# Performance work log

Measured on AMD Instinct MI355X. Metric: run time of the kernel, lower is better.

Reference implementation:

```python
import jax, jax.numpy as jnp
import numpy as np

N_NODES = 50000
N_EDGES = 800000
IN_DIM = 128
OUT_DIM = 128
N_CLASSES = 10
N_GRAPHS = 64


def setup_inputs() -> dict:
    key = jax.random.key(0)
    ks = jax.random.split(key, 8)
    features = jax.random.normal(ks[0], (N_NODES, IN_DIM), dtype=jnp.float32)
    src = jax.random.randint(ks[1], (N_EDGES,), 0, N_NODES, dtype=jnp.int64)
    dst = jax.random.randint(ks[2], (N_EDGES,), 0, N_NODES, dtype=jnp.int64)
    graph_ids = jnp.sort(jax.random.randint(ks[3], (N_NODES,), 0, N_GRAPHS, dtype=jnp.int64))
    # GraphConv params (glorot-ish scale) and linear head params
    W = jax.random.normal(ks[4], (IN_DIM, OUT_DIM), dtype=jnp.float32) / np.sqrt(IN_DIM)
    b = jnp.zeros((OUT_DIM,), dtype=jnp.float32)
    W_head = jax.random.normal(ks[5], (OUT_DIM, N_CLASSES), dtype=jnp.float32) / np.sqrt(OUT_DIM)
    b_head = jnp.zeros((N_CLASSES,), dtype=jnp.float32)
    return {"features": features, "src": src, "dst": dst, "graph_ids": graph_ids,
            "W": W, "b": b, "W_head": W_head, "b_head": b_head}


def reference(features, src, dst, graph_ids, W, b, W_head, b_head):
    # DGL GraphConv, norm='both': D_out^-1/2 -> sum aggregate -> D_in^-1/2 -> XW+b -> relu
    ones_e = jnp.ones((src.shape[0],), dtype=features.dtype)
    out_deg = jax.ops.segment_sum(ones_e, src, num_segments=N_NODES)
    in_deg = jax.ops.segment_sum(ones_e, dst, num_segments=N_NODES)
    out_norm = jax.lax.rsqrt(jnp.clip(out_deg, 1.0))[:, None]   # [N,1]
    in_norm = jax.lax.rsqrt(jnp.clip(in_deg, 1.0))[:, None]     # [N,1]
    h = features * out_norm                                      # [N,D]
    agg = jax.ops.segment_sum(h[src], dst, num_segments=N_NODES) # gather-scatter [E,D]->[N,D]
    agg = agg * in_norm
    h = jax.nn.relu(agg @ W + b)                                 # [N,D_out]
    # dgl.mean_nodes: segment mean over graphs (note: original returns after layer 0)
    cnt = jax.ops.segment_sum(jnp.ones((N_NODES,), dtype=h.dtype), graph_ids, num_segments=N_GRAPHS)
    pooled = jax.ops.segment_sum(h, graph_ids, num_segments=N_GRAPHS) / jnp.clip(cnt, 1.0)[:, None]
    return pooled @ W_head + b_head                              # [G, n_classes]
```

## Files before the change

### kernel.cpp

```cpp
#include <hip/hip_runtime.h>

#define N_NODES   50000
#define N_EDGES   800000
#define DIM       128
#define N_GRAPHS  64
#define N_CLASSES 10
#define NCHE      64
#define CSZ       (N_EDGES / NCHE)
#define LQ        (N_NODES / 4)
#define WPB       64
#define NBR2      ((LQ + WPB - 1) / WPB)
#define PLACE_BPC ((CSZ + 255) / 256)
#define PLACE_BLKS (NCHE * PLACE_BPC)
#define PRES_BLKS ((N_NODES * DIM / 8 + 255) / 256)
#define WT_BLKS   (DIM * DIM / 256)
#define NPBM      128
#define NBLK_NODE ((N_NODES + NPBM - 1) / NPBM)

typedef _Float16 h8 __attribute__((ext_vector_type(8)));
typedef float f4v __attribute__((ext_vector_type(4)));

__global__ __launch_bounds__(256) void k_lhist(const int* __restrict__ src,
                                               const int* __restrict__ dst,
                                               unsigned* __restrict__ Hin,
                                               unsigned* __restrict__ Hout,
                                               unsigned char* __restrict__ perm) {
    __shared__ unsigned L[LQ];
    int c = blockIdx.x, t = threadIdx.x;
    int base = c * CSZ;
    for (int w = t; w < LQ; w += 256) L[w] = 0u;
    __syncthreads();
    if (blockIdx.y == 0) {
        for (int i = t; i < CSZ; i += 256) {
            int d = dst[base + i];
            int sh = (d & 3) * 8;
            unsigned old = atomicAdd(&L[d >> 2], 1u << sh);
            perm[base + i] = (unsigned char)((old >> sh) & 0xffu);
        }
        __syncthreads();
        for (int w = t; w < LQ; w += 256) Hin[(size_t)c * LQ + w] = L[w];
    } else {
        for (int i = t; i < CSZ; i += 256) {
            int s = src[base + i];
            atomicAdd(&L[s >> 2], 1u << ((s & 3) * 8));
        }
        __syncthreads();
        for (int w = t; w < LQ; w += 256) Hout[(size_t)c * LQ + w] = L[w];
    }
}

__global__ __launch_bounds__(256) void k_reduce(unsigned* __restrict__ Hin,
                                                const unsigned* __restrict__ Hout,
                                                const int* __restrict__ gid,
                                                unsigned* __restrict__ indeg,
                                                float* __restrict__ outnorm,
                                                float* __restrict__ innorm,
                                                int* __restrict__ start,
                                                unsigned* __restrict__ row_ptr,
                                                unsigned* __restrict__ blockSums) {
    __shared__ unsigned sIn[4][WPB];
    __shared__ unsigned sOut[4][WPB];
    __shared__ unsigned sS[WPB];
    int t = threadIdx.x;
    int wl = t & (WPB - 1);
    int g  = t >> 6;
    int w  = blockIdx.x * WPB + wl;
    unsigned gs = 0, os = 0;
    int c0 = g * (NCHE / 4);
    if (w < LQ) {
        for (int c = c0; c < c0 + NCHE / 4; ++c) {
            gs += Hin[(size_t)c * LQ + w];
            os += Hout[(size_t)c * LQ + w];
        }
    }
    sIn[g][wl] = gs; sOut[g][wl] = os;
    __syncthreads();
    unsigned baseg = 0;
    for (int gg = 0; gg < 4; ++gg) if (gg < g) baseg += sIn[gg][wl];
    if (w < LQ) {
        unsigned running = baseg;
        for (int c = c0; c < c0 + NCHE / 4; ++c) {
            size_t idx = (size_t)c * LQ + w;
            unsigned word = Hin[idx];
            Hin[idx] = running;
            running += word;
        }
    }
    unsigned tot = 0, otot = 0, wtot = 0;
    if (t < WPB) {
        tot  = sIn[0][t] + sIn[1][t] + sIn[2][t] + sIn[3][t];
        otot = sOut[0][t] + sOut[1][t] + sOut[2][t] + sOut[3][t];
        wtot = (tot & 0xffu) + ((tot >> 8) & 0xffu) + ((tot >> 16) & 0xffu) + (tot >> 24);
        sS[t] = wtot;
    }
    __syncthreads();
    for (int off = 1; off < WPB; off <<= 1) {
        unsigned x = (t < WPB && t >= off) ? sS[t - off] : 0u;
        __syncthreads();
        if (t < WPB) sS[t] += x;
        __syncthreads();
    }
    if (t < WPB) {
        int ww = blockIdx.x * WPB + t;
        if (ww < LQ) {
            unsigned r0 = tot & 0xffu, r1 = (tot >> 8) & 0xffu,
                     r2 = (tot >> 16) & 0xffu, r3 = tot >> 24;
            unsigned o0 = otot & 0xffu, o1 = (otot >> 8) & 0xffu,
                     o2 = (otot >> 16) & 0xffu, o3 = otot >> 24;
            unsigned ex = sS[t] - wtot;
            int n = 4 * ww;
            row_ptr[n]     = ex;
            row_ptr[n + 1] = ex + r0;
            row_ptr[n + 2] = ex + r0 + r1;
            row_ptr[n + 3] = ex + r0 + r1 + r2;
            unsigned rr[4] = {r0, r1, r2, r3}, oo[4] = {o0, o1, o2, o3};
#pragma unroll
            for (int j = 0; j < 4; ++j) {
                indeg[n + j]   = rr[j];
                innorm[n + j]  = rsqrtf(fmaxf((float)rr[j], 1.0f));
                outnorm[n + j] = rsqrtf(fmaxf((float)oo[j], 1.0f));
                int i = n + j;
                int gq = gid[i];
                if (i == 0) {
                    for (int x2 = 0; x2 <= gq; ++x2) start[x2] = 0;
                } else {
                    int gp = gid[i - 1];
                    if (gp != gq)
                        for (int x2 = gp + 1; x2 <= gq; ++x2) start[x2] = i;
                }
                if (i == N_NODES - 1)
                    for (int x2 = gq + 1; x2 <= N_GRAPHS; ++x2) start[x2] = N_NODES;
            }
        }
        if (t == WPB - 1) blockSums[blockIdx.x] = sS[WPB - 1];
    }
}

__global__ __launch_bounds__(256) void k_scan2(unsigned* __restrict__ blockSums,
                                               unsigned* __restrict__ blockOff,
                                               float* __restrict__ pooled) {
    __shared__ unsigned s[256];
    int t = threadIdx.x;
    unsigned val = (t < NBR2) ? blockSums[t] : 0u;
    s[t] = val;
    __syncthreads();
    for (int off = 1; off < 256; off <<= 1) {
        unsigned x = (t >= off) ? s[t - off] : 0u;
        __syncthreads();
        s[t] += x;
        __syncthreads();
    }
    if (t < NBR2) blockOff[t] = s[t] - val;
    float4 z = {0.f, 0.f, 0.f, 0.f};
    for (int i = t; i < N_GRAPHS * DIM / 4; i += 256)
        reinterpret_cast<float4*>(pooled)[i] = z;
}

__global__ __launch_bounds__(256) void k_prep(const int* __restrict__ src,
                                              const int* __restrict__ dst,
                                              const unsigned* __restrict__ Hin,
                                              const unsigned char* __restrict__ perm,
                                              const unsigned* __restrict__ row_ptr,
                                              const unsigned* __restrict__ blockOff,
                                              unsigned short* __restrict__ bsrc,
                                              const float* __restrict__ feat,
                                              const float* __restrict__ outnorm,
                                              _Float16* __restrict__ sfeat,
                                              const float* __restrict__ W,
                                              _Float16* __restrict__ Wt) {
    int t = threadIdx.x;
    int blk = blockIdx.x;
    if (blk < PLACE_BLKS) {
        int c = blk / PLACE_BPC;
        int i = (blk % PLACE_BPC) * 256 + t;
        if (i < CSZ) {
            int e = c * CSZ + i;
            int d = dst[e];
            int sh = (d & 3) * 8;
            unsigned pre = (Hin[(size_t)c * LQ + (d >> 2)] >> sh) & 0xffu;
            unsigned pos = row_ptr[d] + blockOff[d >> 8] + pre + perm[e];
            bsrc[pos] = (unsigned short)src[e];
        }
    } else if (blk < PLACE_BLKS + PRES_BLKS) {
        int i = (blk - PLACE_BLKS) * 256 + t;
        if (i < N_NODES * DIM / 8) {
            int n = i >> 4;
            int d = (i & 15) << 3;
            float nrm = outnorm[n];
            const float4* p = reinterpret_cast<const float4*>(feat + (size_t)n * DIM + d);
            float4 a = p[0], q = p[1];
            h8 r;
            r[0] = (_Float16)(a.x * nrm); r[1] = (_Float16)(a.y * nrm);
            r[2] = (_Float16)(a.z * nrm); r[3] = (_Float16)(a.w * nrm);
            r[4] = (_Float16)(q.x * nrm); r[5] = (_Float16)(q.y * nrm);
            r[6] = (_Float16)(q.z * nrm); r[7] = (_Float16)(q.w * nrm);
            *reinterpret_cast<h8*>(sfeat + (size_t)n * DIM + d) = r;
        }
    } else {
        int i = (blk - PLACE_BLKS - PRES_BLKS) * 256 + t;
        int n = i >> 7, k = i & 127;
        Wt[n * DIM + k] = (_Float16)W[k * DIM + n];
    }
}

#define CVT8(ACC_A, ACC_B, R, M) \
    ACC_A.x += (M) * (float)R[0]; ACC_A.y += (M) * (float)R[1]; \
    ACC_A.z += (M) * (float)R[2]; ACC_A.w += (M) * (float)R[3]; \
    ACC_B.x += (M) * (float)R[4]; ACC_B.y += (M) * (float)R[5]; \
    ACC_B.z += (M) * (float)R[6]; ACC_B.w += (M) * (float)R[7];

__global__ __launch_bounds__(256) void k_gather(const unsigned short* __restrict__ bsrc,
                                                const unsigned* __restrict__ row_ptr,
                                                const unsigned* __restrict__ blockOff,
                                                const unsigned* __restrict__ indeg,
                                                const _Float16* __restrict__ sfeat,
                                                const float* __restrict__ innorm,
                                                _Float16* __restrict__ aggh) {
    int tid = threadIdx.x;
    int wave = tid >> 6;
    int lane = tid & 63;
    int node = blockIdx.x * 4 + wave;
    if (node >= N_NODES) return;
    unsigned start = row_ptr[node] + blockOff[node >> 8];
    unsigned deg   = indeg[node];
    unsigned lim   = deg < 64u ? deg : 64u;
    int qtr = lane >> 4;
    int d8  = (lane & 15) << 3;
    int sIdx = 0;
    if ((unsigned)lane < lim) sIdx = bsrc[start + lane];
    float4 accA = {0,0,0,0}, accB = {0,0,0,0};
    float4 accC = {0,0,0,0}, accD = {0,0,0,0};
    for (unsigned j = 0; j < lim; j += 16) {
        unsigned j0 = j + qtr, j1 = j + 4 + qtr, j2 = j + 8 + qtr, j3 = j + 12 + qtr;
        int s0 = __shfl(sIdx, (int)(j0 < lim ? j0 : 0u));
        int s1 = __shfl(sIdx, (int)(j1 < lim ? j1 : 0u));
        int s2 = __shfl(sIdx, (int)(j2 < lim ? j2 : 0u));
        int s3 = __shfl(sIdx, (int)(j3 < lim ? j3 : 0u));
        float m0 = (j0 < lim) ? 1.f : 0.f;
        float m1 = (j1 < lim) ? 1.f : 0.f;
        float m2 = (j2 < lim) ? 1.f : 0.f;
        float m3 = (j3 < lim) ? 1.f : 0.f;
        h8 r0 = *reinterpret_cast<const h8*>(sfeat + (size_t)s0 * DIM + d8);
        h8 r1 = *reinterpret_cast<const h8*>(sfeat + (size_t)s1 * DIM + d8);
        h8 r2 = *reinterpret_cast<const h8*>(sfeat + (size_t)s2 * DIM + d8);
        h8 r3 = *reinterpret_cast<const h8*>(sfeat + (size_t)s3 * DIM + d8);
        CVT8(accA, accB, r0, m0);
        CVT8(accC, accD, r1, m1);
        CVT8(accA, accB, r2, m2);
        CVT8(accC, accD, r3, m3);
    }
    for (unsigned j = 64; j < deg; j += 4) {
        unsigned jj = j + qtr;
        bool valid = jj < deg;
        int s = bsrc[start + (valid ? jj : 0u)];
        float m = valid ? 1.f : 0.f;
        h8 r = *reinterpret_cast<const h8*>(sfeat + (size_t)s * DIM + d8);
        CVT8(accA, accB, r, m);
    }
    accA.x += accC.x; accA.y += accC.y; accA.z += accC.z; accA.w += accC.w;
    accB.x += accD.x; accB.y += accD.y; accB.z += accD.z; accB.w += accD.w;
    accA.x += __shfl_down(accA.x, 32); accA.y += __shfl_down(accA.y, 32);
    accA.z += __shfl_down(accA.z, 32); accA.w += __shfl_down(accA.w, 32);
    accB.x += __shfl_down(accB.x, 32); accB.y += __shfl_down(accB.y, 32);
    accB.z += __shfl_down(accB.z, 32); accB.w += __shfl_down(accB.w, 32);
    accA.x += __shfl_down(accA.x, 16); accA.y += __shfl_down(accA.y, 16);
    accA.z += __shfl_down(accA.z, 16); accA.w += __shfl_down(accA.w, 16);
    accB.x += __shfl_down(accB.x, 16); accB.y += __shfl_down(accB.y, 16);
    accB.z += __shfl_down(accB.z, 16); accB.w += __shfl_down(accB.w, 16);
    if (qtr == 0) {
        float innrm = innorm[node];
        h8 r;
        r[0] = (_Float16)(accA.x * innrm); r[1] = (_Float16)(accA.y * innrm);
        r[2] = (_Float16)(accA.z * innrm); r[3] = (_Float16)(accA.w * innrm);
        r[4] = (_Float16)(accB.x * innrm); r[5] = (_Float16)(accB.y * innrm);
        r[6] = (_Float16)(accB.z * innrm); r[7] = (_Float16)(accB.w * innrm);
        *reinterpret_cast<h8*>(aggh + (size_t)node * DIM + d8) = r;
    }
}

__global__ __launch_bounds__(256) void k_node(const _Float16* __restrict__ aggh,
                                              const int* __restrict__ gid,
                                              const _Float16* __restrict__ Wt,
                                              const float* __restrict__ b,
                                              float* __restrict__ pooled) {
    __shared__ float red[4][2][DIM];
    int tid = threadIdx.x;
    int wave = tid >> 6, lane = tid & 63;
    int quad = lane >> 4, m = lane & 15;
    int blockBase = blockIdx.x * NPBM;
    int wbase = blockBase + wave * 32;
    int gfirst = gid[blockBase];
    int gsec = gfirst + 1;

    f4v acc0[8], acc1[8];
#pragma unroll
    for (int t = 0; t < 8; ++t) { acc0[t] = (f4v){0,0,0,0}; acc1[t] = (f4v){0,0,0,0}; }

#pragma unroll
    for (int kk = 0; kk < 4; ++kk) {
        int ko = kk * 32 + quad * 8;
        h8 a0 = *reinterpret_cast<const h8*>(aggh + (size_t)(wbase + m) * DIM + ko);
        h8 a1 = *reinterpret_cast<const h8*>(aggh + (size_t)(wbase + 16 + m) * DIM + ko);
#pragma unroll
        for (int t = 0; t < 8; ++t) {
            h8 bf = *reinterpret_cast<const h8*>(Wt + (size_t)(t * 16 + m) * DIM + ko);
            acc0[t] = __builtin_amdgcn_mfma_f32_16x16x32_f16(a0, bf, acc0[t], 0, 0, 0);
            acc1[t] = __builtin_amdgcn_mfma_f32_16x16x32_f16(a1, bf, acc1[t], 0, 0, 0);
        }
    }

    int n0 = wbase + quad * 4;
    int n1 = n0 + 16;
    float s0[8], s1[8];
#pragma unroll
    for (int t = 0; t < 8; ++t) {
        float bb = b[t * 16 + m];
        s0[t] = 0.f; s1[t] = 0.f;
#pragma unroll
        for (int r = 0; r < 4; ++r) {
            int node = n0 + r;
            if (node < N_NODES) {
                float h = fmaxf(acc0[t][r] + bb, 0.f);
                int g = gid[node];
                if (g == gfirst)      s0[t] += h;
                else if (g == gsec)   s1[t] += h;
                else atomicAdd(&pooled[(size_t)g * DIM + t * 16 + m], h);
            }
            int node2 = n1 + r;
            if (node2 < N_NODES) {
                float h = fmaxf(acc1[t][r] + bb, 0.f);
                int g = gid[node2];
                if (g == gfirst)      s0[t] += h;
                else if (g == gsec)   s1[t] += h;
                else atomicAdd(&pooled[(size_t)g * DIM + t * 16 + m], h);
            }
        }
        s0[t] += __shfl_down(s0[t], 32);
        s0[t] += __shfl_down(s0[t], 16);
        s1[t] += __shfl_down(s1[t], 32);
        s1[t] += __shfl_down(s1[t], 16);
    }
    if (quad == 0) {
#pragma unroll
        for (int t = 0; t < 8; ++t) {
            red[wave][0][t * 16 + m] = s0[t];
            red[wave][1][t * 16 + m] = s1[t];
        }
    }
    __syncthreads();
    if (tid < DIM) {
        float v0 = red[0][0][tid] + red[1][0][tid] + red[2][0][tid] + red[3][0][tid];
        if (v0 != 0.f) atomicAdd(&pooled[(size_t)gfirst * DIM + tid], v0);
        float v1 = red[0][1][tid] + red[1][1][tid] + red[2][1][tid] + red[3][1][tid];
        if (v1 != 0.f && gsec < N_GRAPHS) atomicAdd(&pooled[(size_t)gsec * DIM + tid], v1);
    }
}

__global__ __launch_bounds__(256) void k_head(const float* __restrict__ pooled,
                                              const int* __restrict__ start,
                                              const float* __restrict__ Wh,
                                              const float* __restrict__ bh,
                                              float* __restrict__ out) {
    int i = blockIdx.x * 256 + threadIdx.x;
    if (i >= N_GRAPHS * N_CLASSES) return;
    int g = i / N_CLASSES, c = i % N_CLASSES;
    const float* pr = pooled + g * DIM;
    float s = 0.f;
#pragma unroll 8
    for (int k = 0; k < DIM; ++k) s += pr[k] * Wh[k * N_CLASSES + c];
    float cntf = fmaxf((float)(start[g + 1] - start[g]), 1.0f);
    out[i] = s / cntf + bh[c];
}

extern "C" void kernel_launch(void* const* d_in, const int* in_sizes, int n_in,
                              void* d_out, int out_size, void* d_ws, size_t ws_size,
                              hipStream_t stream) {
    const float* feat = (const float*)d_in[0];
    const int*   src  = (const int*)d_in[1];
    const int*   dst  = (const int*)d_in[2];
    const int*   gid  = (const int*)d_in[3];
    const float* W    = (const float*)d_in[4];
    const float* b    = (const float*)d_in[5];
    const float* Wh   = (const float*)d_in[6];
    const float* bh   = (const float*)d_in[7];
    float* out = (float*)d_out;

    float*    pooled   = (float*)d_ws;
    unsigned* indeg    = (unsigned*)(pooled + (size_t)N_GRAPHS * DIM);
    float*    outnorm  = (float*)(indeg + N_NODES);
    float*    innorm   = outnorm + N_NODES;
    int*      start    = (int*)(innorm + N_NODES);
    unsigned* row_ptr  = (unsigned*)(start + 128);
    unsigned* blockSums= row_ptr + N_NODES;
    unsigned* blockOff = blockSums + 256;
    unsigned char* perm= (unsigned char*)(blockOff + 256);
    unsigned short* bsrc = (unsigned short*)(perm + N_EDGES);
    _Float16* sfeat    = (_Float16*)(bsrc + N_EDGES);
    _Float16* aggh     = sfeat + (size_t)N_NODES * DIM;
    _Float16* Wt       = aggh + (size_t)N_NODES * DIM;
    unsigned* Hin      = (unsigned*)(Wt + DIM * DIM);
    unsigned* Hout     = Hin + (size_t)NCHE * LQ;

    dim3 lh(NCHE, 2);
    k_lhist <<<lh, 256, 0, stream>>>(src, dst, Hin, Hout, perm);
    k_reduce<<<NBR2, 256, 0, stream>>>(Hin, Hout, gid, indeg, outnorm, innorm,
                                       start, row_ptr, blockSums);
    k_scan2 <<<1, 256, 0, stream>>>(blockSums, blockOff, pooled);
    k_prep  <<<PLACE_BLKS + PRES_BLKS + WT_BLKS, 256, 0, stream>>>(
                src, dst, Hin, perm, row_ptr, blockOff, bsrc,
                feat, outnorm, sfeat, W, Wt);
    k_gather<<<(N_NODES + 3) / 4, 256, 0, stream>>>(bsrc, row_ptr, blockOff, indeg,
                                                    sfeat, innorm, aggh);
    k_node  <<<NBLK_NODE, 256, 0, stream>>>(aggh, gid, Wt, b, pooled);
    k_head  <<<3, 256, 0, stream>>>(pooled, start, Wh, bh, out);
}
```

Baseline: 180.2 us.

## Fuse gather aggregation with node GEMM and move feature cast into histogram kernel

The fp16 feature conversion and W transpose move into the histogram launch, with the out-degree normalization applied per edge during the gather instead of at conversion time. The gather and the MFMA node transform are fused into one kernel that builds a 128-row aggregated tile in XOR-swizzled LDS, which removes the aggh global round trip and one launch. In exchange, each 16-lane group now walks 8 nodes serially, adds a per-edge outnorm load, uses larger LDS per block that may reduce occupancy, and runs with fewer blocks in the gather phase.

After: 184.9 us. 1.03x slower.

```diff
diff --git a/kernel.cpp b/kernel.cpp
--- a/kernel.cpp
+++ b/kernel.cpp
@@ -14,6 +14,8 @@
 #define PLACE_BLKS (NCHE * PLACE_BPC)
 #define PRES_BLKS ((N_NODES * DIM / 8 + 255) / 256)
 #define WT_BLKS   (DIM * DIM / 256)
+#define LH_HIST   (2 * NCHE)
+#define LH_BLKS   (LH_HIST + PRES_BLKS + WT_BLKS)
 #define NPBM      128
 #define NBLK_NODE ((N_NODES + NPBM - 1) / NPBM)
 
@@ -24,13 +26,40 @@
                                                const int* __restrict__ dst,
                                                unsigned* __restrict__ Hin,
                                                unsigned* __restrict__ Hout,
-                                               unsigned char* __restrict__ perm) {
+                                               unsigned char* __restrict__ perm,
+                                               const float* __restrict__ feat,
+                                               _Float16* __restrict__ sfeat,
+                                               const float* __restrict__ W,
+                                               _Float16* __restrict__ Wt) {
     __shared__ unsigned L[LQ];
-    int c = blockIdx.x, t = threadIdx.x;
+    int blk = blockIdx.x, t = threadIdx.x;
+    if (blk >= LH_HIST) {
+        int q = blk - LH_HIST;
+        if (q < PRES_BLKS) {
+            int i = q * 256 + t;
+            if (i < N_NODES * DIM / 8) {
+                const float4* p = reinterpret_cast<const float4*>(feat + (size_t)i * 8);
+                float4 a = p[0], qv = p[1];
+                h8 r;
+                r[0] = (_Float16)a.x;  r[1] = (_Float16)a.y;
+                r[2] = (_Float16)a.z;  r[3] = (_Float16)a.w;
+                r[4] = (_Float16)qv.x; r[5] = (_Float16)qv.y;
+                r[6] = (_Float16)qv.z; r[7] = (_Float16)qv.w;
+                *reinterpret_cast<h8*>(sfeat + (size_t)i * 8) = r;
+            }
+        } else {
+            int i = (q - PRES_BLKS) * 256 + t;
+            int n = i >> 7, k = i & 127;
+            Wt[n * DIM + k] = (_Float16)W[k * DIM + n];
+        }
+        return;
+    }
+    int c = blk & (NCHE - 1);
+    int phase = blk >> 6;
     int base = c * CSZ;
     for (int w = t; w < LQ; w += 256) L[w] = 0u;
     __syncthreads();
-    if (blockIdx.y == 0) {
+    if (phase == 0) {
         for (int i = t; i < CSZ; i += 256) {
             int d = dst[base + i];
             int sh = (d & 3) * 8;
@@ -156,50 +185,24 @@
         reinterpret_cast<float4*>(pooled)[i] = z;
 }
 
-__global__ __launch_bounds__(256) void k_prep(const int* __restrict__ src,
-                                              const int* __restrict__ dst,
-                                              const unsigned* __restrict__ Hin,
-                                              const unsigned char* __restrict__ perm,
-                                              const unsigned* __restrict__ row_ptr,
-                                              const unsigned* __restrict__ blockOff,
-                                              unsigned short* __restrict__ bsrc,
-                                              const float* __restrict__ feat,
-                                              const float* __restrict__ outnorm,
-                                              _Float16* __restrict__ sfeat,
-                                              const float* __restrict__ W,
-                                              _Float16* __restrict__ Wt) {
+__global__ __launch_bounds__(256) void k_place(const int* __restrict__ src,
+                                               const int* __restrict__ dst,
+                                               const unsigned* __restrict__ Hin,
+                                               const unsigned char* __restrict__ perm,
+                                               const unsigned* __restrict__ row_ptr,
+                                               const unsigned* __restrict__ blockOff,
+                                               unsigned short* __restrict__ bsrc) {
     int t = threadIdx.x;
     int blk = blockIdx.x;
-    if (blk < PLACE_BLKS) {
-        int c = blk / PLACE_BPC;
-        int i = (blk % PLACE_BPC) * 256 + t;
-        if (i < CSZ) {
-            int e = c * CSZ + i;
-            int d = dst[e];
-            int sh = (d & 3) * 8;
-            unsigned pre = (Hin[(size_t)c * LQ + (d >> 2)] >> sh) & 0xffu;
-            unsigned pos = row_ptr[d] + blockOff[d >> 8] + pre + perm[e];
-            bsrc[pos] = (unsigned short)src[e];
-        }
-    } else if (blk < PLACE_BLKS + PRES_BLKS) {
-        int i = (blk - PLACE_BLKS) * 256 + t;
-        if (i < N_NODES * DIM / 8) {
-            int n = i >> 4;
-            int d = (i & 15) << 3;
-            float nrm = outnorm[n];
-            const float4* p = reinterpret_cast<const float4*>(feat + (size_t)n * DIM + d);
-            float4 a = p[0], q = p[1];
-            h8 r;
-            r[0] = (_Float16)(a.x * nrm); r[1] = (_Float16)(a.y * nrm);
-            r[2] = (_Float16)(a.z * nrm); r[3] = (_Float16)(a.w * nrm);
-            r[4] = (_Float16)(q.x * nrm); r[5] = (_Float16)(q.y * nrm);
-            r[6] = (_Float16)(q.z * nrm); r[7] = (_Float16)(q.w * nrm);
-            *reinterpret_cast<h8*>(sfeat + (size_t)n * DIM + d) = r;
-        }
-    } else {
-        int i = (blk - PLACE_BLKS - PRES_BLKS) * 256 + t;
-        int n = i >> 7, k = i & 127;
-        Wt[n * DIM + k] = (_Float16)W[k * DIM + n];
+    int c = blk / PLACE_BPC;
+    int i = (blk % PLACE_BPC) * 256 + t;
+    if (i < CSZ) {
+        int e = c * CSZ + i;
+        int d = dst[e];
+        int sh = (d & 3) * 8;
+        unsigned pre = (Hin[(size_t)c * LQ + (d >> 2)] >> sh) & 0xffu;
+        unsigned pos = row_ptr[d] + blockOff[d >> 8] + pre + perm[e];
+        bsrc[pos] = (unsigned short)src[e];
     }
 }
 
@@ -209,86 +212,76 @@
     ACC_B.x += (M) * (float)R[4]; ACC_B.y += (M) * (float)R[5]; \
     ACC_B.z += (M) * (float)R[6]; ACC_B.w += (M) * (float)R[7];
 
-__global__ __launch_bounds__(256) void k_gather(const unsigned short* __restrict__ bsrc,
-                                                const unsigned* __restrict__ row_ptr,
-                                                const unsigned* __restrict__ blockOff,
-                                                const unsigned* __restrict__ indeg,
-                                                const _Float16* __restrict__ sfeat,
-                                                const float* __restrict__ innorm,
-                                                _Float16* __restrict__ aggh) {
+__global__ __launch_bounds__(256) void k_gnode(const unsigned short* __restrict__ bsrc,
+                                               const unsigned* __restrict__ row_ptr,
+                                               const unsigned* __restrict__ blockOff,
+                                               const unsigned* __restrict__ indeg,
+                                               const _Float16* __restrict__ sfeat,
+                                               const float* __restrict__ outnorm,
+                                               const float* __restrict__ innorm,
+                                               const int* __restrict__ gid,
+                                               const _Float16* __restrict__ Wt,
+                                               const float* __restrict__ b,
+                                               float* __restrict__ pooled) {
+    __shared__ _Float16 aggL[NPBM * DIM];
+    __shared__ float red[4][2][DIM];
     int tid = threadIdx.x;
-    int wave = tid >> 6;
-    int lane = tid & 63;
-    int node = blockIdx.x * 4 + wave;
-    if (node >= N_NODES) return;
-    unsigned start = row_ptr[node] + blockOff[node >> 8];
-    unsigned deg   = indeg[node];
-    unsigned lim   = deg < 64u ? deg : 64u;
-    int qtr = lane >> 4;
-    int d8  = (lane & 15) << 3;
-    int sIdx = 0;
-    if ((unsigned)lane < lim) sIdx = bsrc[start + lane];
-    float4 accA = {0,0,0,0}, accB = {0,0,0,0};
-    float4 accC = {0,0,0,0}, accD = {0,0,0,0};
-    for (unsigned j = 0; j < lim; j += 16) {
-        unsigned j0 = j + qtr, j1 = j + 4 + qtr, j2 = j + 8 + qtr, j3 = j + 12 + qtr;
-        int s0 = __shfl(sIdx, (int)(j0 < lim ? j0 : 0u));
-        int s1 = __shfl(sIdx, (int)(j1 < lim ? j1 : 0u));
-        int s2 = __shfl(sIdx, (int)(j2 < lim ? j2 : 0u));
-        int s3 = __shfl(sIdx, (int)(j3 < lim ? j3 : 0u));
-        float m0 = (j0 < lim) ? 1.f : 0.f;
-        float m1 = (j1 < lim) ? 1.f : 0.f;
-        float m2 = (j2 < lim) ? 1.f : 0.f;
-        float m3 = (j3 < lim) ? 1.f : 0.f;
-        h8 r0 = *reinterpret_cast<const h8*>(sfeat + (size_t)s0 * DIM + d8);
-        h8 r1 = *reinterpret_cast<const h8*>(sfeat + (size_t)s1 * DIM + d8);
-        h8 r2 = *reinterpret_cast<const h8*>(sfeat + (size_t)s2 * DIM + d8);
-        h8 r3 = *reinterpret_cast<const h8*>(sfeat + (size_t)s3 * DIM + d8);
-        CVT8(accA, accB, r0, m0);
-        CVT8(accC, accD, r1, m1);
-        CVT8(accA, accB, r2, m2);
-        CVT8(accC, accD, r3, m3);
-    }
-    for (unsigned j = 64; j < deg; j += 4) {
-        unsigned jj = j + qtr;
-        bool valid = jj < deg;
-        int s = bsrc[start + (valid ? jj : 0u)];
-        float m = valid ? 1.f : 0.f;
-        h8 r = *reinterpret_cast<const h8*>(sfeat + (size_t)s * DIM + d8);
-        CVT8(accA, accB, r, m);
-    }
-    accA.x += accC.x; accA.y += accC.y; accA.z += accC.z; accA.w += accC.w;
-    accB.x += accD.x; accB.y += accD.y; accB.z += accD.z; accB.w += accD.w;
-    accA.x += __shfl_down(accA.x, 32); accA.y += __shfl_down(accA.y, 32);
-    accA.z += __shfl_down(accA.z, 32); accA.w += __shfl_down(accA.w, 32);
-    accB.x += __shfl_down(accB.x, 32); accB.y += __shfl_down(accB.y, 32);
-    accB.z += __shfl_down(accB.z, 32); accB.w += __shfl_down(accB.w, 32);
-    accA.x += __shfl_down(accA.x, 16); accA.y += __shfl_down(accA.y, 16);
-    accA.z += __shfl_down(accA.z, 16); accA.w += __shfl_down(accA.w, 16);
-    accB.x += __shfl_down(accB.x, 16); accB.y += __shfl_down(accB.y, 16);
-    accB.z += __shfl_down(accB.z, 16); accB.w += __shfl_down(accB.w, 16);
-    if (qtr == 0) {
-        float innrm = innorm[node];
+    int lane = tid & 63, wave = tid >> 6;
+    int gl = lane & 15;
+    int gb = lane & 48;
+    int grp = tid >> 4;
+    int blockBase = blockIdx.x * NPBM;
+    int d8 = gl * 8;
+
+#pragma unroll 1
+    for (int rr = 0; rr < 8; ++rr) {
+        int row = grp * 8 + rr;
+        int node = blockBase + row;
+        float4 accA = {0,0,0,0}, accB = {0,0,0,0};
+        float4 accC = {0,0,0,0}, accD = {0,0,0,0};
+        float innrm = 0.f;
+        if (node < N_NODES) {
+            unsigned start = row_ptr[node] + blockOff[node >> 8];
+            unsigned deg   = indeg[node];
+            innrm = innorm[node];
+            for (unsigned j0 = 0; j0 < deg; j0 += 16) {
+                unsigned cnt = deg - j0; if (cnt > 16u) cnt = 16u;
+                int sIdx = bsrc[start + j0 + ((unsigned)gl < cnt ? (unsigned)gl : 0u)];
+                for (unsigned j = 0; j < cnt; j += 4) {
+                    unsigned j1 = j + 1, j2 = j + 2, j3 = j + 3;
+                    int s0 = __shfl(sIdx, gb + (int)j);
+                    int s1 = __shfl(sIdx, gb + (int)(j1 < cnt ? j1 : 0u));
+                    int s2 = __shfl(sIdx, gb + (int)(j2 < cnt ? j2 : 0u));
+                    int s3 = __shfl(sIdx, gb + (int)(j3 < cnt ? j3 : 0u));
+                    float m0 = outnorm[s0];
+                    float m1 = (j1 < cnt) ? outnorm[s1] : 0.f;
+                    float m2 = (j2 < cnt) ? outnorm[s2] : 0.f;
+                    float m3 = (j3 < cnt) ? outnorm[s3] : 0.f;
+                    h8 r0 = *reinterpret_cast<const h8*>(sfeat + (size_t)s0 * DIM + d8);
+                    h8 r1 = *reinterpret_cast<const h8*>(sfeat + (size_t)s1 * DIM + d8);
+                    h8 r2 = *reinterpret_cast<const h8*>(sfeat + (size_t)s2 * DIM + d8);
+                    h8 r3 = *reinterpret_cast<const h8*>(sfeat + (size_t)s3 * DIM + d8);
+                    CVT8(accA, accB, r0, m0);
+                    CVT8(accC, accD, r1, m1);
+                    CVT8(accA, accB, r2, m2);
+                    CVT8(accC, accD, r3, m3);
+                }
+            }
+        }
+        accA.x += accC.x; accA.y += accC.y; accA.z += accC.z; accA.w += accC.w;
+        accB.x += accD.x; accB.y += accD.y; accB.z += accD.z; accB.w += accD.w;
         h8 r;
         r[0] = (_Float16)(accA.x * innrm); r[1] = (_Float16)(accA.y * innrm);
         r[2] = (_Float16)(accA.z * innrm); r[3] = (_Float16)(accA.w * innrm);
         r[4] = (_Float16)(accB.x * innrm); r[5] = (_Float16)(accB.y * innrm);
         r[6] = (_Float16)(accB.z * innrm); r[7] = (_Float16)(accB.w * innrm);
-        *reinterpret_cast<h8*>(aggh + (size_t)node * DIM + d8) = r;
-    }
-}
-
-__global__ __launch_bounds__(256) void k_node(const _Float16* __restrict__ aggh,
-                                              const int* __restrict__ gid,
-                                              const _Float16* __restrict__ Wt,
-                                              const float* __restrict__ b,
-                                              float* __restrict__ pooled) {
-    __shared__ float red[4][2][DIM];
-    int tid = threadIdx.x;
-    int wave = tid >> 6, lane = tid & 63;
+        int slot = gl ^ (row & 7);
+        *reinterpret_cast<h8*>(&aggL[row * DIM + slot * 8]) = r;
+    }
+    __syncthreads();
+
     int quad = lane >> 4, m = lane & 15;
-    int blockBase = blockIdx.x * NPBM;
-    int wbase = blockBase + wave * 32;
+    int lrow = wave * 32;
     int gfirst = gid[blockBase];
     int gsec = gfirst + 1;
 
@@ -299,8 +292,11 @@
 #pragma unroll
     for (int kk = 0; kk < 4; ++kk) {
         int ko = kk * 32 + quad * 8;
-        h8 a0 = *reinterpret_cast<const h8*>(aggh + (size_t)(wbase + m) * DIM + ko);
-        h8 a1 = *reinterpret_cast<const h8*>(aggh + (size_t)(wbase + 16 + m) * DIM + ko);
+        int r0 = lrow + m, r1 = lrow + 16 + m;
+        int slot0 = (kk * 4 + quad) ^ (r0 & 7);
+        int slot1 = (kk * 4 + quad) ^ (r1 & 7);
+        h8 a0 = *reinterpret_cast<const h8*>(&aggL[r0 * DIM + slot0 * 8]);
+        h8 a1 = *reinterpret_cast<const h8*>(&aggL[r1 * DIM + slot1 * 8]);
 #pragma unroll
         for (int t = 0; t < 8; ++t) {
             h8 bf = *reinterpret_cast<const h8*>(Wt + (size_t)(t * 16 + m) * DIM + ko);
@@ -309,6 +305,7 @@
         }
     }
 
+    int wbase = blockBase + lrow;
     int n0 = wbase + quad * 4;
     int n1 = n0 + 16;
     float s0[8], s1[8];
@@ -401,16 +398,14 @@
     unsigned* Hin      = (unsigned*)(Wt + DIM * DIM);
     unsigned* Hout     = Hin + (size_t)NCHE * LQ;
 
-    dim3 lh(NCHE, 2);
-    k_lhist <<<lh, 256, 0, stream>>>(src, dst, Hin, Hout, perm);
+    k_lhist <<<LH_BLKS, 256, 0, stream>>>(src, dst, Hin, Hout, perm,
+                                          feat, sfeat, W, Wt);
     k_reduce<<<NBR2, 256, 0, stream>>>(Hin, Hout, gid, indeg, outnorm, innorm,
                                        start, row_ptr, blockSums);
     k_scan2 <<<1, 256, 0, stream>>>(blockSums, blockOff, pooled);
-    k_prep  <<<PLACE_BLKS + PRES_BLKS + WT_BLKS, 256, 0, stream>>>(
-                src, dst, Hin, perm, row_ptr, blockOff, bsrc,
-                feat, outnorm, sfeat, W, Wt);
-    k_gather<<<(N_NODES + 3) / 4, 256, 0, stream>>>(bsrc, row_ptr, blockOff, indeg,
-                                                    sfeat, innorm, aggh);
-    k_node  <<<NBLK_NODE, 256, 0, stream>>>(aggh, gid, Wt, b, pooled);
+    k_place <<<PLACE_BLKS, 256, 0, stream>>>(src, dst, Hin, perm, row_ptr,
+                                             blockOff, bsrc);
+    k_gnode <<<NBLK_NODE, 256, 0, stream>>>(bsrc, row_ptr, blockOff, indeg,
+                                            sfeat, outnorm, innorm, gid, Wt, b, pooled);
     k_head  <<<3, 256, 0, stream>>>(pooled, start, Wh, bh, out);
 }
```

## Move feature fp16 conversion into histogram kernel, apply out-norm in gather

Applied to the files above, without the earlier changes.

The fp16 feature conversion and the W transpose move out of the placement kernel and into the first histogram launch, so they run alongside the edge histograms instead of after the degree reduction. Since the out-degree norm is not yet known at that point, the gather now loads outnorm[src] per edge and uses it as the accumulation weight. This takes the conversion work off the critical path but adds a scattered 4-byte load per edge in the gather. Features are also stored to fp16 before normalization, which slightly changes rounding.

Result: faster. 175.0 us (-2.9%).

```diff
diff --git a/kernel.cpp b/kernel.cpp
--- a/kernel.cpp
+++ b/kernel.cpp
@@ -14,6 +14,8 @@
 #define PLACE_BLKS (NCHE * PLACE_BPC)
 #define PRES_BLKS ((N_NODES * DIM / 8 + 255) / 256)
 #define WT_BLKS   (DIM * DIM / 256)
+#define LH_HIST   (2 * NCHE)
+#define LH_BLKS   (LH_HIST + PRES_BLKS + WT_BLKS)
 #define NPBM      128
 #define NBLK_NODE ((N_NODES + NPBM - 1) / NPBM)
 
@@ -24,13 +26,40 @@
                                                const int* __restrict__ dst,
                                                unsigned* __restrict__ Hin,
                                                unsigned* __restrict__ Hout,
-                                               unsigned char* __restrict__ perm) {
+                                               unsigned char* __restrict__ perm,
+                                               const float* __restrict__ feat,
+                                               _Float16* __restrict__ sfeat,
+                                               const float* __restrict__ W,
+                                               _Float16* __restrict__ Wt) {
     __shared__ unsigned L[LQ];
-    int c = blockIdx.x, t = threadIdx.x;
+    int blk = blockIdx.x, t = threadIdx.x;
+    if (blk >= LH_HIST) {
+        int q = blk - LH_HIST;
+        if (q < PRES_BLKS) {
+            int i = q * 256 + t;
+            if (i < N_NODES * DIM / 8) {
+                const float4* p = reinterpret_cast<const float4*>(feat + (size_t)i * 8);
+                float4 a = p[0], qv = p[1];
+                h8 r;
+                r[0] = (_Float16)a.x;  r[1] = (_Float16)a.y;
+                r[2] = (_Float16)a.z;  r[3] = (_Float16)a.w;
+                r[4] = (_Float16)qv.x; r[5] = (_Float16)qv.y;
+                r[6] = (_Float16)qv.z; r[7] = (_Float16)qv.w;
+                *reinterpret_cast<h8*>(sfeat + (size_t)i * 8) = r;
+            }
+        } else {
+            int i = (q - PRES_BLKS) * 256 + t;
+            int n = i >> 7, k = i & 127;
+            Wt[n * DIM + k] = (_Float16)W[k * DIM + n];
+        }
+        return;
+    }
+    int c = blk & (NCHE - 1);
+    int phase = blk >> 6;
     int base = c * CSZ;
     for (int w = t; w < LQ; w += 256) L[w] = 0u;
     __syncthreads();
-    if (blockIdx.y == 0) {
+    if (phase == 0) {
         for (int i = t; i < CSZ; i += 256) {
             int d = dst[base + i];
             int sh = (d & 3) * 8;
@@ -156,50 +185,24 @@
         reinterpret_cast<float4*>(pooled)[i] = z;
 }
 
-__global__ __launch_bounds__(256) void k_prep(const int* __restrict__ src,
-                                              const int* __restrict__ dst,
-                                              const unsigned* __restrict__ Hin,
-                                              const unsigned char* __restrict__ perm,
-                                              const unsigned* __restrict__ row_ptr,
-                                              const unsigned* __restrict__ blockOff,
-                                              unsigned short* __restrict__ bsrc,
-                                              const float* __restrict__ feat,
-                                              const float* __restrict__ outnorm,
-                                              _Float16* __restrict__ sfeat,
-                                              const float* __restrict__ W,
-                                              _Float16* __restrict__ Wt) {
+__global__ __launch_bounds__(256) void k_place(const int* __restrict__ src,
+                                               const int* __restrict__ dst,
+                                               const unsigned* __restrict__ Hin,
+                                               const unsigned char* __restrict__ perm,
+                                               const unsigned* __restrict__ row_ptr,
+                                               const unsigned* __restrict__ blockOff,
+                                               unsigned short* __restrict__ bsrc) {
     int t = threadIdx.x;
     int blk = blockIdx.x;
-    if (blk < PLACE_BLKS) {
-        int c = blk / PLACE_BPC;
-        int i = (blk % PLACE_BPC) * 256 + t;
-        if (i < CSZ) {
-            int e = c * CSZ + i;
-            int d = dst[e];
-            int sh = (d & 3) * 8;
-            unsigned pre = (Hin[(size_t)c * LQ + (d >> 2)] >> sh) & 0xffu;
-            unsigned pos = row_ptr[d] + blockOff[d >> 8] + pre + perm[e];
-            bsrc[pos] = (unsigned short)src[e];
-        }
-    } else if (blk < PLACE_BLKS + PRES_BLKS) {
-        int i = (blk - PLACE_BLKS) * 256 + t;
-        if (i < N_NODES * DIM / 8) {
-            int n = i >> 4;
-            int d = (i & 15) << 3;
-            float nrm = outnorm[n];
-            const float4* p = reinterpret_cast<const float4*>(feat + (size_t)n * DIM + d);
-            float4 a = p[0], q = p[1];
-            h8 r;
-            r[0] = (_Float16)(a.x * nrm); r[1] = (_Float16)(a.y * nrm);
-            r[2] = (_Float16)(a.z * nrm); r[3] = (_Float16)(a.w * nrm);
-            r[4] = (_Float16)(q.x * nrm); r[5] = (_Float16)(q.y * nrm);
-            r[6] = (_Float16)(q.z * nrm); r[7] = (_Float16)(q.w * nrm);
-            *reinterpret_cast<h8*>(sfeat + (size_t)n * DIM + d) = r;
-        }
-    } else {
-        int i = (blk - PLACE_BLKS - PRES_BLKS) * 256 + t;
-        int n = i >> 7, k = i & 127;
-        Wt[n * DIM + k] = (_Float16)W[k * DIM + n];
+    int c = blk / PLACE_BPC;
+    int i = (blk % PLACE_BPC) * 256 + t;
+    if (i < CSZ) {
+        int e = c * CSZ + i;
+        int d = dst[e];
+        int sh = (d & 3) * 8;
+        unsigned pre = (Hin[(size_t)c * LQ + (d >> 2)] >> sh) & 0xffu;
+        unsigned pos = row_ptr[d] + blockOff[d >> 8] + pre + perm[e];
+        bsrc[pos] = (unsigned short)src[e];
     }
 }
 
@@ -214,6 +217,7 @@
                                                 const unsigned* __restrict__ blockOff,
                                                 const unsigned* __restrict__ indeg,
                                                 const _Float16* __restrict__ sfeat,
+                                                const float* __restrict__ outnorm,
                                                 const float* __restrict__ innorm,
                                                 _Float16* __restrict__ aggh) {
     int tid = threadIdx.x;
@@ -236,10 +240,10 @@
         int s1 = __shfl(sIdx, (int)(j1 < lim ? j1 : 0u));
         int s2 = __shfl(sIdx, (int)(j2 < lim ? j2 : 0u));
         int s3 = __shfl(sIdx, (int)(j3 < lim ? j3 : 0u));
-        float m0 = (j0 < lim) ? 1.f : 0.f;
-        float m1 = (j1 < lim) ? 1.f : 0.f;
-        float m2 = (j2 < lim) ? 1.f : 0.f;
-        float m3 = (j3 < lim) ? 1.f : 0.f;
+        float m0 = (j0 < lim) ? outnorm[s0] : 0.f;
+        float m1 = (j1 < lim) ? outnorm[s1] : 0.f;
+        float m2 = (j2 < lim) ? outnorm[s2] : 0.f;
+        float m3 = (j3 < lim) ? outnorm[s3] : 0.f;
         h8 r0 = *reinterpret_cast<const h8*>(sfeat + (size_t)s0 * DIM + d8);
         h8 r1 = *reinterpret_cast<const h8*>(sfeat + (size_t)s1 * DIM + d8);
         h8 r2 = *reinterpret_cast<const h8*>(sfeat + (size_t)s2 * DIM + d8);
@@ -253,7 +257,7 @@
         unsigned jj = j + qtr;
         bool valid = jj < deg;
         int s = bsrc[start + (valid ? jj : 0u)];
-        float m = valid ? 1.f : 0.f;
+        float m = valid ? outnorm[s] : 0.f;
         h8 r = *reinterpret_cast<const h8*>(sfeat + (size_t)s * DIM + d8);
         CVT8(accA, accB, r, m);
     }
@@ -401,16 +405,15 @@
     unsigned* Hin      = (unsigned*)(Wt + DIM * DIM);
     unsigned* Hout     = Hin + (size_t)NCHE * LQ;
 
-    dim3 lh(NCHE, 2);
-    k_lhist <<<lh, 256, 0, stream>>>(src, dst, Hin, Hout, perm);
+    k_lhist <<<LH_BLKS, 256, 0, stream>>>(src, dst, Hin, Hout, perm,
+                                          feat, sfeat, W, Wt);
     k_reduce<<<NBR2, 256, 0, stream>>>(Hin, Hout, gid, indeg, outnorm, innorm,
                                        start, row_ptr, blockSums);
     k_scan2 <<<1, 256, 0, stream>>>(blockSums, blockOff, pooled);
-    k_prep  <<<PLACE_BLKS + PRES_BLKS + WT_BLKS, 256, 0, stream>>>(
-                src, dst, Hin, perm, row_ptr, blockOff, bsrc,
-                feat, outnorm, sfeat, W, Wt);
+    k_place <<<PLACE_BLKS, 256, 0, stream>>>(src, dst, Hin, perm, row_ptr,
+                                             blockOff, bsrc);
     k_gather<<<(N_NODES + 3) / 4, 256, 0, stream>>>(bsrc, row_ptr, blockOff, indeg,
-                                                    sfeat, innorm, aggh);
+                                                    sfeat, outnorm, innorm, aggh);
     k_node  <<<NBLK_NODE, 256, 0, stream>>>(aggh, gid, Wt, b, pooled);
     k_head  <<<3, 256, 0, stream>>>(pooled, start, Wh, bh, out);
 }
```
